# Optimization experiments

Hardware: AMD Instinct MI355X
Metric: run time of the kernel (lower is better)

Reference implementation:

```python
import jax, jax.numpy as jnp
import numpy as np

HEADS = 4

def setup_inputs() -> dict:
    B, L, D = 4, 2048, 256
    key = jax.random.key(0)
    k1, k2, k3, k4, k5, k6 = jax.random.split(key, 6)
    return {
        "atten": jax.random.normal(k1, (B, L, L), dtype=jnp.float32),
        "value": jax.random.normal(k2, (B, L, D), dtype=jnp.float32),
        "mask": jax.random.uniform(k3, (B, 1, L, L), dtype=jnp.float32),
        "padding_mask": jax.random.randint(k4, (B, L, L), 0, 2, dtype=jnp.int32),
        "Wv": jax.random.normal(k5, (D, D), dtype=jnp.float32) * 0.02,
        "bv": jnp.zeros((D,), dtype=jnp.float32),
        "Wo": jax.random.normal(k6, (D, D), dtype=jnp.float32) * 0.02,
        "bo": jnp.zeros((D,), dtype=jnp.float32),
    }

def reference(atten, value, mask, padding_mask, Wv, bv, Wo, bo):
    B, L, D = value.shape
    H = HEADS
    dk = D // H
    # to_value: Linear then split heads. N == 1 (value.unsqueeze(1) in torch).
    v = value @ Wv + bv                                   # (B, L, D)
    v = v.reshape(B, 1, L, H, dk).transpose(0, 3, 1, 2, 4)  # (B, H, N=1, L, dk)
    # externally supplied attention logits, two sequential masked fills
    a = atten[:, None, :, :]                              # (B, 1, L, L)
    a = jnp.where(mask < 0.5, jnp.finfo(a.dtype).min, a)
    a = jnp.where(padding_mask[:, None, :, :] == 0, -jnp.inf, a)
    a = jax.nn.softmax(a, axis=-1)                        # (B, 1, L, L)
    # dropout is identity in eval mode
    # einsum 'bhij,bhnjk->bhnik' with h=1 on a broadcast across H heads of v
    out = jnp.einsum('bij,bhnjk->bhnik', a[:, 0], v)      # (B, H, 1, L, dk)
    out = out.transpose(0, 2, 3, 1, 4).reshape(B, 1, L, D)
    out = out @ Wo + bo                                   # (B, 1, L, D)
    return out
```

## Files before the change

kernel.cpp:

```cpp
#include <hip/hip_runtime.h>
#include <hip/hip_bf16.h>
#include <math.h>

#define L 2048
#define D 256

typedef __attribute__((ext_vector_type(8))) short bf16x8;
typedef __attribute__((ext_vector_type(4))) float f32x4;
typedef __attribute__((ext_vector_type(4))) int i32x4;

__device__ __forceinline__ unsigned short f2bf(float f) {
    union { float f; unsigned int u; } v; v.f = f;
    unsigned int r = v.u + 0x7FFFu + ((v.u >> 16) & 1u);
    return (unsigned short)(r >> 16);
}

__global__ __launch_bounds__(256) void wtrans_kernel(
    const float* __restrict__ Wv, const float* __restrict__ Wo,
    unsigned short* __restrict__ Wvt, unsigned short* __restrict__ Wot) {
    int idx = blockIdx.x * 256 + threadIdx.x;
    int which = idx >> 16;
    int e = idx & 65535;
    int n = e >> 8, k = e & 255;
    const float* W = which ? Wo : Wv;
    unsigned short* Wt = which ? Wot : Wvt;
    Wt[n * 256 + k] = f2bf(W[k * 256 + n]);
}

__global__ __launch_bounds__(256) void gemm_v_kernel(
    const float* __restrict__ A,
    const unsigned short* __restrict__ Wt,
    const float* __restrict__ bias,
    unsigned short* __restrict__ Vt) {
    const int wave = threadIdx.x >> 6;
    const int lane = threadIdx.x & 63;
    const int mh = wave >> 1, nh = wave & 1;
    const int lm = lane & 15, q = lane >> 4;
    const int m0 = blockIdx.x * 64;
    const int n0 = blockIdx.y * 128;

    f32x4 acc[2][4];
#pragma unroll
    for (int i = 0; i < 2; i++)
#pragma unroll
        for (int j = 0; j < 4; j++) acc[i][j] = (f32x4)(0.f);

    int arow[2];
    arow[0] = m0 + mh * 32 + lm;
    arow[1] = arow[0] + 16;
    int ncol[4];
#pragma unroll
    for (int nf = 0; nf < 4; nf++) ncol[nf] = n0 + nh * 64 + nf * 16 + lm;

    for (int k0 = 0; k0 < 256; k0 += 32) {
        int kq = k0 + q * 8;
        bf16x8 bfr[4];
#pragma unroll
        for (int nf = 0; nf < 4; nf++)
            bfr[nf] = *reinterpret_cast<const bf16x8*>(Wt + ncol[nf] * 256 + kq);
        bf16x8 afr[2];
#pragma unroll
        for (int mf = 0; mf < 2; mf++) {
            const float* ap = A + arow[mf] * 256 + kq;
            f32x4 a0 = *reinterpret_cast<const f32x4*>(ap);
            f32x4 a1 = *reinterpret_cast<const f32x4*>(ap + 4);
            bf16x8 t;
#pragma unroll
            for (int e = 0; e < 4; e++) t[e] = (short)f2bf(a0[e]);
#pragma unroll
            for (int e = 0; e < 4; e++) t[4 + e] = (short)f2bf(a1[e]);
            afr[mf] = t;
        }
#pragma unroll
        for (int mf = 0; mf < 2; mf++)
#pragma unroll
            for (int nf = 0; nf < 4; nf++)
                acc[mf][nf] = __builtin_amdgcn_mfma_f32_16x16x32_bf16(
                    afr[mf], bfr[nf], acc[mf][nf], 0, 0, 0);
    }

#pragma unroll
    for (int mf = 0; mf < 2; mf++) {
        int mrow = m0 + mh * 32 + mf * 16 + q * 4;
#pragma unroll
        for (int nf = 0; nf < 4; nf++) {
            int n = ncol[nf];
            float bias_n = bias[n];
            int b = mrow >> 11;
            int j = mrow & 2047;
            unsigned short* dst = Vt + (size_t)b * (D * L) + (size_t)n * L + j;
            ushort4 pk;
            pk.x = f2bf(acc[mf][nf][0] + bias_n);
            pk.y = f2bf(acc[mf][nf][1] + bias_n);
            pk.z = f2bf(acc[mf][nf][2] + bias_n);
            pk.w = f2bf(acc[mf][nf][3] + bias_n);
            *reinterpret_cast<ushort4*>(dst) = pk;
        }
    }
}

__global__ __launch_bounds__(256) void attn_kernel(
    const float* __restrict__ atten, const float* __restrict__ mask,
    const int* __restrict__ pad, const unsigned short* __restrict__ Vt,
    float* __restrict__ part) {
    const int blk = blockIdx.x;
    const int rb = blk >> 2, js = blk & 3;
    const int b = rb >> 6;
    const int i0 = (rb & 63) * 32;
    const int tid = threadIdx.x;
    const int wave = tid >> 6, lane = tid & 63;
    const int lm = lane & 15, q = lane >> 4;
    const int r = tid >> 3;
    const int c0 = (tid & 7) * 8;

    __shared__ __align__(16) unsigned short Plds[2][32][72];

    f32x4 acc[2][4];
#pragma unroll
    for (int i = 0; i < 2; i++)
#pragma unroll
        for (int j = 0; j < 4; j++) acc[i][j] = (f32x4)(0.f);
    float l_th = 0.f;

    const size_t rowoff = ((size_t)(b * L + i0 + r)) * L + js * 512 + c0;
    const float* at_row = atten + rowoff;
    const float* mk_row = mask + rowoff;
    const int* pd_row = pad + rowoff;
    const unsigned short* vt_b = Vt + (size_t)b * (D * L) + js * 512;

    f32x4 ca0 = *reinterpret_cast<const f32x4*>(at_row);
    f32x4 ca1 = *reinterpret_cast<const f32x4*>(at_row + 4);
    f32x4 ck0 = *reinterpret_cast<const f32x4*>(mk_row);
    f32x4 ck1 = *reinterpret_cast<const f32x4*>(mk_row + 4);
    i32x4 cp0 = *reinterpret_cast<const i32x4*>(pd_row);
    i32x4 cp1 = *reinterpret_cast<const i32x4*>(pd_row + 4);

    for (int jt = 0; jt < 8; jt++) {
        const int j0 = jt * 64;
        f32x4 na0, na1, nk0, nk1; i32x4 np0, np1;
        if (jt < 7) {
            const int jn = j0 + 64;
            na0 = *reinterpret_cast<const f32x4*>(at_row + jn);
            na1 = *reinterpret_cast<const f32x4*>(at_row + jn + 4);
            nk0 = *reinterpret_cast<const f32x4*>(mk_row + jn);
            nk1 = *reinterpret_cast<const f32x4*>(mk_row + jn + 4);
            np0 = *reinterpret_cast<const i32x4*>(pd_row + jn);
            np1 = *reinterpret_cast<const i32x4*>(pd_row + jn + 4);
        }
        bf16x8 bfr[2][4];
#pragma unroll
        for (int kk = 0; kk < 2; kk++)
#pragma unroll
            for (int nf = 0; nf < 4; nf++) {
                int n = wave * 64 + nf * 16 + lm;
                bfr[kk][nf] = *reinterpret_cast<const bf16x8*>(
                    vt_b + (size_t)n * L + j0 + kk * 32 + q * 8);
            }
        bf16x8 pk;
        float psum = 0.f;
#pragma unroll
        for (int e = 0; e < 4; e++) {
            float pv = (ck0[e] < 0.5f || cp0[e] == 0) ? 0.f : __expf(ca0[e]);
            float pw = (ck1[e] < 0.5f || cp1[e] == 0) ? 0.f : __expf(ca1[e]);
            psum += pv + pw;
            pk[e] = (short)f2bf(pv);
            pk[4 + e] = (short)f2bf(pw);
        }
        l_th += psum;

        const int par = jt & 1;
        *reinterpret_cast<bf16x8*>(&Plds[par][r][c0]) = pk;
        __syncthreads();

#pragma unroll
        for (int kk = 0; kk < 2; kk++)
#pragma unroll
            for (int mf = 0; mf < 2; mf++) {
                bf16x8 afr = *reinterpret_cast<const bf16x8*>(
                    &Plds[par][mf * 16 + lm][kk * 32 + q * 8]);
#pragma unroll
                for (int nf = 0; nf < 4; nf++)
                    acc[mf][nf] = __builtin_amdgcn_mfma_f32_16x16x32_bf16(
                        afr, bfr[kk][nf], acc[mf][nf], 0, 0, 0);
            }
        ca0 = na0; ca1 = na1; ck0 = nk0; ck1 = nk1; cp0 = np0; cp1 = np1;
    }

#pragma unroll
    for (int off = 1; off < 8; off <<= 1) l_th += __shfl_xor(l_th, off);

    float* pbase = part + (size_t)blk * 8224;
#pragma unroll
    for (int mf = 0; mf < 2; mf++)
#pragma unroll
        for (int nf = 0; nf < 4; nf++) {
            int n = wave * 64 + nf * 16 + lm;
#pragma unroll
            for (int rg = 0; rg < 4; rg++)
                pbase[(mf * 16 + q * 4 + rg) * 256 + n] = acc[mf][nf][rg];
        }
    if ((tid & 7) == 0) pbase[8192 + r] = l_th;
}

__global__ __launch_bounds__(256) void combine_gemm_kernel(
    const float* __restrict__ part, const unsigned short* __restrict__ Wot,
    const float* __restrict__ bo, float* __restrict__ out) {
    const int rb = blockIdx.x;
    const int tid = threadIdx.x;
    const int wave = tid >> 6, lane = tid & 63;
    const int lm = lane & 15, q = lane >> 4;
    const int r = tid >> 3;
    const int n0 = (tid & 7) * 32;

    __shared__ __align__(16) unsigned short Alds[32][264];

    const float* pb = part + (size_t)(rb * 4) * 8224;
    float l = pb[8192 + r] + pb[8224 + 8192 + r] +
              pb[2 * 8224 + 8192 + r] + pb[3 * 8224 + 8192 + r];
    float inv = 1.f / l;
#pragma unroll
    for (int e = 0; e < 32; e += 4) {
        f32x4 s = (f32x4)(0.f);
#pragma unroll
        for (int js = 0; js < 4; js++)
            s += *reinterpret_cast<const f32x4*>(pb + js * 8224 + r * 256 + n0 + e);
        s *= inv;
        ushort4 pk;
        pk.x = f2bf(s[0]); pk.y = f2bf(s[1]); pk.z = f2bf(s[2]); pk.w = f2bf(s[3]);
        *reinterpret_cast<ushort4*>(&Alds[r][n0 + e]) = pk;
    }
    __syncthreads();

    f32x4 acc[2][4];
#pragma unroll
    for (int i = 0; i < 2; i++)
#pragma unroll
        for (int j = 0; j < 4; j++) acc[i][j] = (f32x4)(0.f);
    int ncol[4];
#pragma unroll
    for (int nf = 0; nf < 4; nf++) ncol[nf] = wave * 64 + nf * 16 + lm;

    for (int kk = 0; kk < 8; kk++) {
        int kq = kk * 32 + q * 8;
        bf16x8 bfr[4];
#pragma unroll
        for (int nf = 0; nf < 4; nf++)
            bfr[nf] = *reinterpret_cast<const bf16x8*>(Wot + ncol[nf] * 256 + kq);
#pragma unroll
        for (int mf = 0; mf < 2; mf++) {
            bf16x8 afr = *reinterpret_cast<const bf16x8*>(&Alds[mf * 16 + lm][kq]);
#pragma unroll
            for (int nf = 0; nf < 4; nf++)
                acc[mf][nf] = __builtin_amdgcn_mfma_f32_16x16x32_bf16(
                    afr, bfr[nf], acc[mf][nf], 0, 0, 0);
        }
    }

#pragma unroll
    for (int mf = 0; mf < 2; mf++) {
        int mrow = rb * 32 + mf * 16 + q * 4;
#pragma unroll
        for (int nf = 0; nf < 4; nf++) {
            int n = ncol[nf];
            float bn = bo[n];
#pragma unroll
            for (int rg = 0; rg < 4; rg++)
                out[(size_t)(mrow + rg) * 256 + n] = acc[mf][nf][rg] + bn;
        }
    }
}

extern "C" void kernel_launch(void* const* d_in, const int* in_sizes, int n_in,
                              void* d_out, int out_size, void* d_ws, size_t ws_size,
                              hipStream_t stream) {
    (void)in_sizes; (void)n_in; (void)out_size; (void)ws_size;
    const float* atten = (const float*)d_in[0];
    const float* value = (const float*)d_in[1];
    const float* mask  = (const float*)d_in[2];
    const int*   pad   = (const int*)d_in[3];
    const float* Wv    = (const float*)d_in[4];
    const float* bv    = (const float*)d_in[5];
    const float* Wo    = (const float*)d_in[6];
    const float* bo    = (const float*)d_in[7];
    float* out = (float*)d_out;

    char* ws = (char*)d_ws;
    unsigned short* Vt  = (unsigned short*)(ws);
    unsigned short* Wvt = (unsigned short*)(ws + 4194304);
    unsigned short* Wot = (unsigned short*)(ws + 4325376);
    float* part = (float*)(ws + 4456448);

    wtrans_kernel<<<512, 256, 0, stream>>>(Wv, Wo, Wvt, Wot);
    gemm_v_kernel<<<dim3(128, 2), 256, 0, stream>>>(value, Wvt, bv, Vt);
    attn_kernel<<<1024, 256, 0, stream>>>(atten, mask, pad, Vt, part);
    combine_gemm_kernel<<<256, 256, 0, stream>>>(part, Wot, bo, out);
}
```

Baseline: 256.5 us.

## Load attention probabilities directly in MFMA A-fragment layout, drop LDS staging

Each wave now loads its atten/mask/pad elements straight into the MFMA A-operand register layout (16 rows × 64 cols per tile), so the LDS write, __syncthreads and LDS read of the probability tile are removed. Work is re-split so each wave owns a 16-row, 128-column output tile for one of four key-chunks, and the partial results and row sums are written to separate buffers in a new layout that the combine kernel reads. The explicit one-step software prefetch of the next input tile is dropped. Each wave now fetches more V fragments per tile (8 instead of 4), and per-thread global loads are strided across rows, which may reduce coalescing.

```diff
diff --git a/kernel.cpp b/kernel.cpp
--- a/kernel.cpp
+++ b/kernel.cpp
@@ -102,132 +102,117 @@
 __global__ __launch_bounds__(256) void attn_kernel(
     const float* __restrict__ atten, const float* __restrict__ mask,
     const int* __restrict__ pad, const unsigned short* __restrict__ Vt,
-    float* __restrict__ part) {
-    const int blk = blockIdx.x;
-    const int rb = blk >> 2, js = blk & 3;
-    const int b = rb >> 6;
-    const int i0 = (rb & 63) * 32;
-    const int tid = threadIdx.x;
-    const int wave = tid >> 6, lane = tid & 63;
+    float* __restrict__ part_acc, float* __restrict__ part_l) {
+    const int bid = blockIdx.x;
+    const int rt = bid >> 1;
+    const int jh = bid & 1;
+    const int wave = threadIdx.x >> 6;
+    const int lane = threadIdx.x & 63;
+    const int js = jh * 2 + (wave >> 1);
+    const int nh = wave & 1;
+    const int b  = rt >> 7;
+    const int i0 = (rt & 127) << 4;
     const int lm = lane & 15, q = lane >> 4;
-    const int r = tid >> 3;
-    const int c0 = (tid & 7) * 8;
-
-    __shared__ __align__(16) unsigned short Plds[2][32][72];
-
-    f32x4 acc[2][4];
-#pragma unroll
-    for (int i = 0; i < 2; i++)
-#pragma unroll
-        for (int j = 0; j < 4; j++) acc[i][j] = (f32x4)(0.f);
+
+    const size_t rowbase = ((size_t)(b * L + i0 + lm)) * L + js * 512 + q * 8;
+    const float* at = atten + rowbase;
+    const float* mk = mask  + rowbase;
+    const int*   pd = pad   + rowbase;
+    const unsigned short* vb = Vt + (size_t)b * (D * L)
+                             + (size_t)(nh * 128 + lm) * L + js * 512 + q * 8;
+
+    f32x4 acc[8];
+#pragma unroll
+    for (int nf = 0; nf < 8; nf++) acc[nf] = (f32x4)(0.f);
     float l_th = 0.f;
-
-    const size_t rowoff = ((size_t)(b * L + i0 + r)) * L + js * 512 + c0;
-    const float* at_row = atten + rowoff;
-    const float* mk_row = mask + rowoff;
-    const int* pd_row = pad + rowoff;
-    const unsigned short* vt_b = Vt + (size_t)b * (D * L) + js * 512;
-
-    f32x4 ca0 = *reinterpret_cast<const f32x4*>(at_row);
-    f32x4 ca1 = *reinterpret_cast<const f32x4*>(at_row + 4);
-    f32x4 ck0 = *reinterpret_cast<const f32x4*>(mk_row);
-    f32x4 ck1 = *reinterpret_cast<const f32x4*>(mk_row + 4);
-    i32x4 cp0 = *reinterpret_cast<const i32x4*>(pd_row);
-    i32x4 cp1 = *reinterpret_cast<const i32x4*>(pd_row + 4);
 
     for (int jt = 0; jt < 8; jt++) {
         const int j0 = jt * 64;
-        f32x4 na0, na1, nk0, nk1; i32x4 np0, np1;
-        if (jt < 7) {
-            const int jn = j0 + 64;
-            na0 = *reinterpret_cast<const f32x4*>(at_row + jn);
-            na1 = *reinterpret_cast<const f32x4*>(at_row + jn + 4);
-            nk0 = *reinterpret_cast<const f32x4*>(mk_row + jn);
-            nk1 = *reinterpret_cast<const f32x4*>(mk_row + jn + 4);
-            np0 = *reinterpret_cast<const i32x4*>(pd_row + jn);
-            np1 = *reinterpret_cast<const i32x4*>(pd_row + jn + 4);
-        }
-        bf16x8 bfr[2][4];
+        bf16x8 bfr[2][8];
 #pragma unroll
         for (int kk = 0; kk < 2; kk++)
 #pragma unroll
-            for (int nf = 0; nf < 4; nf++) {
-                int n = wave * 64 + nf * 16 + lm;
+            for (int nf = 0; nf < 8; nf++)
                 bfr[kk][nf] = *reinterpret_cast<const bf16x8*>(
-                    vt_b + (size_t)n * L + j0 + kk * 32 + q * 8);
-            }
-        bf16x8 pk;
-        float psum = 0.f;
-#pragma unroll
-        for (int e = 0; e < 4; e++) {
-            float pv = (ck0[e] < 0.5f || cp0[e] == 0) ? 0.f : __expf(ca0[e]);
-            float pw = (ck1[e] < 0.5f || cp1[e] == 0) ? 0.f : __expf(ca1[e]);
-            psum += pv + pw;
-            pk[e] = (short)f2bf(pv);
-            pk[4 + e] = (short)f2bf(pw);
-        }
-        l_th += psum;
-
-        const int par = jt & 1;
-        *reinterpret_cast<bf16x8*>(&Plds[par][r][c0]) = pk;
-        __syncthreads();
-
+                    vb + (size_t)nf * (16 * L) + j0 + kk * 32);
+        f32x4 a_[4], m_[4]; i32x4 p_[4];
+#pragma unroll
+        for (int kk = 0; kk < 2; kk++) {
+            a_[kk * 2]     = *reinterpret_cast<const f32x4*>(at + j0 + kk * 32);
+            a_[kk * 2 + 1] = *reinterpret_cast<const f32x4*>(at + j0 + kk * 32 + 4);
+            m_[kk * 2]     = *reinterpret_cast<const f32x4*>(mk + j0 + kk * 32);
+            m_[kk * 2 + 1] = *reinterpret_cast<const f32x4*>(mk + j0 + kk * 32 + 4);
+            p_[kk * 2]     = *reinterpret_cast<const i32x4*>(pd + j0 + kk * 32);
+            p_[kk * 2 + 1] = *reinterpret_cast<const i32x4*>(pd + j0 + kk * 32 + 4);
+        }
+        bf16x8 afr[2];
+#pragma unroll
+        for (int kk = 0; kk < 2; kk++) {
+            bf16x8 t;
+#pragma unroll
+            for (int h = 0; h < 2; h++)
+#pragma unroll
+                for (int e = 0; e < 4; e++) {
+                    float pv = (m_[kk * 2 + h][e] < 0.5f || p_[kk * 2 + h][e] == 0)
+                                   ? 0.f : __expf(a_[kk * 2 + h][e]);
+                    l_th += pv;
+                    t[h * 4 + e] = (short)f2bf(pv);
+                }
+            afr[kk] = t;
+        }
 #pragma unroll
         for (int kk = 0; kk < 2; kk++)
 #pragma unroll
-            for (int mf = 0; mf < 2; mf++) {
-                bf16x8 afr = *reinterpret_cast<const bf16x8*>(
-                    &Plds[par][mf * 16 + lm][kk * 32 + q * 8]);
-#pragma unroll
-                for (int nf = 0; nf < 4; nf++)
-                    acc[mf][nf] = __builtin_amdgcn_mfma_f32_16x16x32_bf16(
-                        afr, bfr[kk][nf], acc[mf][nf], 0, 0, 0);
-            }
-        ca0 = na0; ca1 = na1; ck0 = nk0; ck1 = nk1; cp0 = np0; cp1 = np1;
-    }
-
-#pragma unroll
-    for (int off = 1; off < 8; off <<= 1) l_th += __shfl_xor(l_th, off);
-
-    float* pbase = part + (size_t)blk * 8224;
-#pragma unroll
-    for (int mf = 0; mf < 2; mf++)
-#pragma unroll
-        for (int nf = 0; nf < 4; nf++) {
-            int n = wave * 64 + nf * 16 + lm;
-#pragma unroll
-            for (int rg = 0; rg < 4; rg++)
-                pbase[(mf * 16 + q * 4 + rg) * 256 + n] = acc[mf][nf][rg];
-        }
-    if ((tid & 7) == 0) pbase[8192 + r] = l_th;
+            for (int nf = 0; nf < 8; nf++)
+                acc[nf] = __builtin_amdgcn_mfma_f32_16x16x32_bf16(
+                    afr[kk], bfr[kk][nf], acc[nf], 0, 0, 0);
+    }
+
+    l_th += __shfl_xor(l_th, 16);
+    l_th += __shfl_xor(l_th, 32);
+
+    float* pb = part_acc + ((size_t)(rt * 4 + js) * 2 + nh) * 2048;
+#pragma unroll
+    for (int nf = 0; nf < 8; nf++)
+#pragma unroll
+        for (int rg = 0; rg < 4; rg++)
+            pb[(q * 4 + rg) * 128 + nf * 16 + lm] = acc[nf][rg];
+    if (nh == 0 && lane < 16)
+        part_l[(rt * 4 + js) * 16 + lm] = l_th;
 }
 
 __global__ __launch_bounds__(256) void combine_gemm_kernel(
-    const float* __restrict__ part, const unsigned short* __restrict__ Wot,
-    const float* __restrict__ bo, float* __restrict__ out) {
+    const float* __restrict__ part_acc, const float* __restrict__ part_l,
+    const unsigned short* __restrict__ Wot, const float* __restrict__ bo,
+    float* __restrict__ out) {
     const int rb = blockIdx.x;
     const int tid = threadIdx.x;
     const int wave = tid >> 6, lane = tid & 63;
     const int lm = lane & 15, q = lane >> 4;
     const int r = tid >> 3;
-    const int n0 = (tid & 7) * 32;
+    const int rt = rb * 2 + (r >> 4);
+    const int rr = r & 15;
+    const int cb = (tid & 7) * 32;
+    const int nh = cb >> 7;
+    const int cl = cb & 127;
 
     __shared__ __align__(16) unsigned short Alds[32][264];
 
-    const float* pb = part + (size_t)(rb * 4) * 8224;
-    float l = pb[8192 + r] + pb[8224 + 8192 + r] +
-              pb[2 * 8224 + 8192 + r] + pb[3 * 8224 + 8192 + r];
+    float l = 0.f;
+#pragma unroll
+    for (int js = 0; js < 4; js++) l += part_l[(rt * 4 + js) * 16 + rr];
     float inv = 1.f / l;
 #pragma unroll
     for (int e = 0; e < 32; e += 4) {
         f32x4 s = (f32x4)(0.f);
 #pragma unroll
         for (int js = 0; js < 4; js++)
-            s += *reinterpret_cast<const f32x4*>(pb + js * 8224 + r * 256 + n0 + e);
+            s += *reinterpret_cast<const f32x4*>(
+                part_acc + ((size_t)(rt * 4 + js) * 2 + nh) * 2048 + rr * 128 + cl + e);
         s *= inv;
         ushort4 pk;
         pk.x = f2bf(s[0]); pk.y = f2bf(s[1]); pk.z = f2bf(s[2]); pk.w = f2bf(s[3]);
-        *reinterpret_cast<ushort4*>(&Alds[r][n0 + e]) = pk;
+        *reinterpret_cast<ushort4*>(&Alds[r][cb + e]) = pk;
     }
     __syncthreads();
 
@@ -288,10 +273,11 @@
     unsigned short* Vt  = (unsigned short*)(ws);
     unsigned short* Wvt = (unsigned short*)(ws + 4194304);
     unsigned short* Wot = (unsigned short*)(ws + 4325376);
-    float* part = (float*)(ws + 4456448);
+    float* part_acc = (float*)(ws + 4456448);
+    float* part_l   = (float*)(ws + 4456448 + 33554432);
 
     wtrans_kernel<<<512, 256, 0, stream>>>(Wv, Wo, Wvt, Wot);
     gemm_v_kernel<<<dim3(128, 2), 256, 0, stream>>>(value, Wvt, bv, Vt);
-    attn_kernel<<<1024, 256, 0, stream>>>(atten, mask, pad, Vt, part);
-    combine_gemm_kernel<<<256, 256, 0, stream>>>(part, Wot, bo, out);
-}
+    attn_kernel<<<1024, 256, 0, stream>>>(atten, mask, pad, Vt, part_acc, part_l);
+    combine_gemm_kernel<<<256, 256, 0, stream>>>(part_acc, part_l, Wot, bo, out);
+}
```

New measurement: 319.2 us. +24.4%, slower.

## Split attention into elementwise P materialization and fused PV+output GEMM

Applied to the files above, without the earlier changes.

Replaces the fused mask/exp/MFMA attention kernel with two stages. A streaming kernel writes masked exp values as bf16 P plus per-row sums. A second kernel does the full-K P·V GEMM per 32-row block with register double-buffering, normalizes, and feeds the output projection. This removes the split-K partial buffer and the combine reduction, but adds a 32 MB bf16 P round trip through memory, and the PV kernel runs only 256 blocks.

```diff
diff --git a/kernel.cpp b/kernel.cpp
--- a/kernel.cpp
+++ b/kernel.cpp
@@ -99,146 +99,126 @@
     }
 }
 
-__global__ __launch_bounds__(256) void attn_kernel(
+__global__ __launch_bounds__(256) void p_kernel(
     const float* __restrict__ atten, const float* __restrict__ mask,
-    const int* __restrict__ pad, const unsigned short* __restrict__ Vt,
-    float* __restrict__ part) {
-    const int blk = blockIdx.x;
-    const int rb = blk >> 2, js = blk & 3;
-    const int b = rb >> 6;
-    const int i0 = (rb & 63) * 32;
-    const int tid = threadIdx.x;
-    const int wave = tid >> 6, lane = tid & 63;
-    const int lm = lane & 15, q = lane >> 4;
-    const int r = tid >> 3;
-    const int c0 = (tid & 7) * 8;
-
-    __shared__ __align__(16) unsigned short Plds[2][32][72];
-
-    f32x4 acc[2][4];
-#pragma unroll
-    for (int i = 0; i < 2; i++)
-#pragma unroll
-        for (int j = 0; j < 4; j++) acc[i][j] = (f32x4)(0.f);
+    const int* __restrict__ pad, unsigned short* __restrict__ P,
+    float* __restrict__ lsum) {
+    const int row = blockIdx.x * 4 + (threadIdx.x >> 6);
+    const int lane = threadIdx.x & 63;
+
+    const float* at = atten + (size_t)row * L;
+    const float* mk = mask  + (size_t)row * L;
+    const int*   pd = pad   + (size_t)row * L;
+    unsigned short* Pr = P + (size_t)row * L;
+
     float l_th = 0.f;
-
-    const size_t rowoff = ((size_t)(b * L + i0 + r)) * L + js * 512 + c0;
-    const float* at_row = atten + rowoff;
-    const float* mk_row = mask + rowoff;
-    const int* pd_row = pad + rowoff;
-    const unsigned short* vt_b = Vt + (size_t)b * (D * L) + js * 512;
-
-    f32x4 ca0 = *reinterpret_cast<const f32x4*>(at_row);
-    f32x4 ca1 = *reinterpret_cast<const f32x4*>(at_row + 4);
-    f32x4 ck0 = *reinterpret_cast<const f32x4*>(mk_row);
-    f32x4 ck1 = *reinterpret_cast<const f32x4*>(mk_row + 4);
-    i32x4 cp0 = *reinterpret_cast<const i32x4*>(pd_row);
-    i32x4 cp1 = *reinterpret_cast<const i32x4*>(pd_row + 4);
-
-    for (int jt = 0; jt < 8; jt++) {
-        const int j0 = jt * 64;
-        f32x4 na0, na1, nk0, nk1; i32x4 np0, np1;
-        if (jt < 7) {
-            const int jn = j0 + 64;
-            na0 = *reinterpret_cast<const f32x4*>(at_row + jn);
-            na1 = *reinterpret_cast<const f32x4*>(at_row + jn + 4);
-            nk0 = *reinterpret_cast<const f32x4*>(mk_row + jn);
-            nk1 = *reinterpret_cast<const f32x4*>(mk_row + jn + 4);
-            np0 = *reinterpret_cast<const i32x4*>(pd_row + jn);
-            np1 = *reinterpret_cast<const i32x4*>(pd_row + jn + 4);
-        }
-        bf16x8 bfr[2][4];
-#pragma unroll
-        for (int kk = 0; kk < 2; kk++)
-#pragma unroll
-            for (int nf = 0; nf < 4; nf++) {
-                int n = wave * 64 + nf * 16 + lm;
-                bfr[kk][nf] = *reinterpret_cast<const bf16x8*>(
-                    vt_b + (size_t)n * L + j0 + kk * 32 + q * 8);
-            }
-        bf16x8 pk;
-        float psum = 0.f;
-#pragma unroll
-        for (int e = 0; e < 4; e++) {
-            float pv = (ck0[e] < 0.5f || cp0[e] == 0) ? 0.f : __expf(ca0[e]);
-            float pw = (ck1[e] < 0.5f || cp1[e] == 0) ? 0.f : __expf(ca1[e]);
-            psum += pv + pw;
-            pk[e] = (short)f2bf(pv);
-            pk[4 + e] = (short)f2bf(pw);
-        }
-        l_th += psum;
-
-        const int par = jt & 1;
-        *reinterpret_cast<bf16x8*>(&Plds[par][r][c0]) = pk;
-        __syncthreads();
-
-#pragma unroll
-        for (int kk = 0; kk < 2; kk++)
-#pragma unroll
-            for (int mf = 0; mf < 2; mf++) {
-                bf16x8 afr = *reinterpret_cast<const bf16x8*>(
-                    &Plds[par][mf * 16 + lm][kk * 32 + q * 8]);
-#pragma unroll
-                for (int nf = 0; nf < 4; nf++)
-                    acc[mf][nf] = __builtin_amdgcn_mfma_f32_16x16x32_bf16(
-                        afr, bfr[kk][nf], acc[mf][nf], 0, 0, 0);
-            }
-        ca0 = na0; ca1 = na1; ck0 = nk0; ck1 = nk1; cp0 = np0; cp1 = np1;
-    }
-
-#pragma unroll
-    for (int off = 1; off < 8; off <<= 1) l_th += __shfl_xor(l_th, off);
-
-    float* pbase = part + (size_t)blk * 8224;
-#pragma unroll
-    for (int mf = 0; mf < 2; mf++)
-#pragma unroll
-        for (int nf = 0; nf < 4; nf++) {
-            int n = wave * 64 + nf * 16 + lm;
-#pragma unroll
-            for (int rg = 0; rg < 4; rg++)
-                pbase[(mf * 16 + q * 4 + rg) * 256 + n] = acc[mf][nf][rg];
-        }
-    if ((tid & 7) == 0) pbase[8192 + r] = l_th;
-}
-
-__global__ __launch_bounds__(256) void combine_gemm_kernel(
-    const float* __restrict__ part, const unsigned short* __restrict__ Wot,
+#pragma unroll
+    for (int c = 0; c < 8; c++) {
+        const int off = c * 256 + lane * 4;
+        f32x4 a = *reinterpret_cast<const f32x4*>(at + off);
+        f32x4 m = *reinterpret_cast<const f32x4*>(mk + off);
+        i32x4 p = *reinterpret_cast<const i32x4*>(pd + off);
+        ushort4 pk;
+        float pv;
+        pv = (m[0] < 0.5f || p[0] == 0) ? 0.f : __expf(a[0]); l_th += pv; pk.x = f2bf(pv);
+        pv = (m[1] < 0.5f || p[1] == 0) ? 0.f : __expf(a[1]); l_th += pv; pk.y = f2bf(pv);
+        pv = (m[2] < 0.5f || p[2] == 0) ? 0.f : __expf(a[2]); l_th += pv; pk.z = f2bf(pv);
+        pv = (m[3] < 0.5f || p[3] == 0) ? 0.f : __expf(a[3]); l_th += pv; pk.w = f2bf(pv);
+        *reinterpret_cast<ushort4*>(Pr + off) = pk;
+    }
+#pragma unroll
+    for (int off = 1; off < 64; off <<= 1) l_th += __shfl_xor(l_th, off);
+    if (lane == 0) lsum[row] = l_th;
+}
+
+__global__ __launch_bounds__(256) void pv_out_kernel(
+    const unsigned short* __restrict__ P, const unsigned short* __restrict__ Vt,
+    const float* __restrict__ lsum, const unsigned short* __restrict__ Wot,
     const float* __restrict__ bo, float* __restrict__ out) {
     const int rb = blockIdx.x;
     const int tid = threadIdx.x;
-    const int wave = tid >> 6, lane = tid & 63;
+    const int w = tid >> 6, lane = tid & 63;
     const int lm = lane & 15, q = lane >> 4;
-    const int r = tid >> 3;
-    const int n0 = (tid & 7) * 32;
+    const int b = rb >> 6;
+    const int row0 = rb * 32;
+
+    const unsigned short* pA = P + (size_t)row0 * L + q * 8;
+    const unsigned short* pB = Vt + (size_t)b * (D * L) + (size_t)(w * 64) * L + q * 8;
+
+    f32x4 acc[2][4];
+#pragma unroll
+    for (int i = 0; i < 2; i++)
+#pragma unroll
+        for (int j = 0; j < 4; j++) acc[i][j] = (f32x4)(0.f);
+
+    bf16x8 Ac[2][2], Bc[2][4], An[2][2], Bn[2][4];
+#pragma unroll
+    for (int kk = 0; kk < 2; kk++) {
+#pragma unroll
+        for (int mf = 0; mf < 2; mf++)
+            Ac[kk][mf] = *reinterpret_cast<const bf16x8*>(pA + (mf * 16 + lm) * L + kk * 32);
+#pragma unroll
+        for (int nf = 0; nf < 4; nf++)
+            Bc[kk][nf] = *reinterpret_cast<const bf16x8*>(pB + (nf * 16 + lm) * L + kk * 32);
+    }
+
+    for (int k0 = 0; k0 < 2048; k0 += 64) {
+        if (k0 + 64 < 2048) {
+            const int kn = k0 + 64;
+#pragma unroll
+            for (int kk = 0; kk < 2; kk++) {
+#pragma unroll
+                for (int mf = 0; mf < 2; mf++)
+                    An[kk][mf] = *reinterpret_cast<const bf16x8*>(
+                        pA + (mf * 16 + lm) * L + kn + kk * 32);
+#pragma unroll
+                for (int nf = 0; nf < 4; nf++)
+                    Bn[kk][nf] = *reinterpret_cast<const bf16x8*>(
+                        pB + (nf * 16 + lm) * L + kn + kk * 32);
+            }
+        }
+#pragma unroll
+        for (int kk = 0; kk < 2; kk++)
+#pragma unroll
+            for (int mf = 0; mf < 2; mf++)
+#pragma unroll
+                for (int nf = 0; nf < 4; nf++)
+                    acc[mf][nf] = __builtin_amdgcn_mfma_f32_16x16x32_bf16(
+                        Ac[kk][mf], Bc[kk][nf], acc[mf][nf], 0, 0, 0);
+#pragma unroll
+        for (int kk = 0; kk < 2; kk++) {
+#pragma unroll
+            for (int mf = 0; mf < 2; mf++) Ac[kk][mf] = An[kk][mf];
+#pragma unroll
+            for (int nf = 0; nf < 4; nf++) Bc[kk][nf] = Bn[kk][nf];
+        }
+    }
 
     __shared__ __align__(16) unsigned short Alds[32][264];
-
-    const float* pb = part + (size_t)(rb * 4) * 8224;
-    float l = pb[8192 + r] + pb[8224 + 8192 + r] +
-              pb[2 * 8224 + 8192 + r] + pb[3 * 8224 + 8192 + r];
-    float inv = 1.f / l;
-#pragma unroll
-    for (int e = 0; e < 32; e += 4) {
-        f32x4 s = (f32x4)(0.f);
-#pragma unroll
-        for (int js = 0; js < 4; js++)
-            s += *reinterpret_cast<const f32x4*>(pb + js * 8224 + r * 256 + n0 + e);
-        s *= inv;
-        ushort4 pk;
-        pk.x = f2bf(s[0]); pk.y = f2bf(s[1]); pk.z = f2bf(s[2]); pk.w = f2bf(s[3]);
-        *reinterpret_cast<ushort4*>(&Alds[r][n0 + e]) = pk;
+#pragma unroll
+    for (int mf = 0; mf < 2; mf++) {
+        float inv[4];
+#pragma unroll
+        for (int rg = 0; rg < 4; rg++)
+            inv[rg] = 1.f / lsum[row0 + mf * 16 + q * 4 + rg];
+#pragma unroll
+        for (int nf = 0; nf < 4; nf++) {
+            int col = w * 64 + nf * 16 + lm;
+#pragma unroll
+            for (int rg = 0; rg < 4; rg++)
+                Alds[mf * 16 + q * 4 + rg][col] = f2bf(acc[mf][nf][rg] * inv[rg]);
+        }
     }
     __syncthreads();
 
-    f32x4 acc[2][4];
+    f32x4 oacc[2][4];
 #pragma unroll
     for (int i = 0; i < 2; i++)
 #pragma unroll
-        for (int j = 0; j < 4; j++) acc[i][j] = (f32x4)(0.f);
+        for (int j = 0; j < 4; j++) oacc[i][j] = (f32x4)(0.f);
     int ncol[4];
 #pragma unroll
-    for (int nf = 0; nf < 4; nf++) ncol[nf] = wave * 64 + nf * 16 + lm;
+    for (int nf = 0; nf < 4; nf++) ncol[nf] = w * 64 + nf * 16 + lm;
 
     for (int kk = 0; kk < 8; kk++) {
         int kq = kk * 32 + q * 8;
@@ -251,21 +231,21 @@
             bf16x8 afr = *reinterpret_cast<const bf16x8*>(&Alds[mf * 16 + lm][kq]);
 #pragma unroll
             for (int nf = 0; nf < 4; nf++)
-                acc[mf][nf] = __builtin_amdgcn_mfma_f32_16x16x32_bf16(
-                    afr, bfr[nf], acc[mf][nf], 0, 0, 0);
+                oacc[mf][nf] = __builtin_amdgcn_mfma_f32_16x16x32_bf16(
+                    afr, bfr[nf], oacc[mf][nf], 0, 0, 0);
         }
     }
 
 #pragma unroll
     for (int mf = 0; mf < 2; mf++) {
-        int mrow = rb * 32 + mf * 16 + q * 4;
+        int mrow = row0 + mf * 16 + q * 4;
 #pragma unroll
         for (int nf = 0; nf < 4; nf++) {
             int n = ncol[nf];
             float bn = bo[n];
 #pragma unroll
             for (int rg = 0; rg < 4; rg++)
-                out[(size_t)(mrow + rg) * 256 + n] = acc[mf][nf][rg] + bn;
+                out[(size_t)(mrow + rg) * 256 + n] = oacc[mf][nf][rg] + bn;
         }
     }
 }
@@ -288,10 +268,11 @@
     unsigned short* Vt  = (unsigned short*)(ws);
     unsigned short* Wvt = (unsigned short*)(ws + 4194304);
     unsigned short* Wot = (unsigned short*)(ws + 4325376);
-    float* part = (float*)(ws + 4456448);
+    unsigned short* P   = (unsigned short*)(ws + 4456448);
+    float* lsum         = (float*)(ws + 38010880);
 
     wtrans_kernel<<<512, 256, 0, stream>>>(Wv, Wo, Wvt, Wot);
     gemm_v_kernel<<<dim3(128, 2), 256, 0, stream>>>(value, Wvt, bv, Vt);
-    attn_kernel<<<1024, 256, 0, stream>>>(atten, mask, pad, Vt, part);
-    combine_gemm_kernel<<<256, 256, 0, stream>>>(part, Wot, bo, out);
-}
+    p_kernel<<<2048, 256, 0, stream>>>(atten, mask, pad, P, lsum);
+    pv_out_kernel<<<256, 256, 0, stream>>>(P, Vt, lsum, Wot, bo, out);
+}
```

New measurement: 279.5 us. +9.0%, slower.
